# Kernel tuning notes

Measured on AMD Instinct MI355X. Metric: run time of the kernel, lower is better.

The kernel has to match this reference:

```python
import jax, jax.numpy as jnp
import numpy as np

B, N, D, H = 8, 1024, 768, 12
HD = D // H  # 64
SCALE = float(np.sqrt(HD))  # NOTE: source MULTIPLIES by sqrt(head_dim)


def setup_inputs() -> dict:
    key = jax.random.key(0)
    k1, k2, k3, k4 = jax.random.split(key, 4)
    x = jax.random.normal(k1, (B, N, D), dtype=jnp.float32)
    w_qkv = jax.random.normal(k2, (3 * D, D), dtype=jnp.float32) * (1.0 / np.sqrt(D))
    w_fc = jax.random.normal(k3, (D, D), dtype=jnp.float32) * (1.0 / np.sqrt(D))
    b_fc = jax.random.normal(k4, (D,), dtype=jnp.float32) * 0.01
    return {"x": x, "w_qkv": w_qkv, "w_fc": w_fc, "b_fc": b_fc}


def reference(x, w_qkv, w_fc, b_fc):
    b, n, d = x.shape
    # qkv projection (torch Linear: y = x @ W.T), no bias
    qkv = jnp.einsum('bnd,ed->bne', x, w_qkv)  # [b, n, 3*D]
    q, k, v = jnp.split(qkv, 3, axis=-1)
    # 'b n (h d) -> b h n d'
    to_heads = lambda t: t.reshape(b, n, H, HD).transpose(0, 2, 1, 3)
    q, k, v = map(to_heads, (q, k, v))
    # NOTE: faithful to source — scale MULTIPLIES and NO softmax is applied
    attn = SCALE * jnp.einsum('bhid,bhjd->bhij', q, k)  # [b, h, n, n]
    out = jnp.einsum('bhij,bhjd->bhid', attn, v)  # [b, h, n, hd]
    out = out.transpose(0, 2, 1, 3).reshape(b, n, H * HD)  # 'b h n d -> b n (h d)'
    out = jnp.einsum('bnd,ed->bne', out, w_fc) + b_fc  # fc (dropout = identity in eval)
    return out
```

## Files before the change

### kernel.cpp

```cpp
#include <hip/hip_runtime.h>
#include <stdint.h>

#define Bb 8
#define Nn 1024
#define Dd 768
#define Hh 12
#define HDd 64
#define Mm (Bb * Nn)
#define QKVN (3 * Dd)
#define SCALE_F 8.0f

typedef __attribute__((ext_vector_type(8))) short bf16x8;
typedef __attribute__((ext_vector_type(4))) float f32x4;

__device__ __forceinline__ float bf2f(unsigned short u) {
  unsigned int v = ((unsigned int)u) << 16;
  float f;
  __builtin_memcpy(&f, &v, 4);
  return f;
}
__device__ __forceinline__ unsigned short f2bf(float f) {
  unsigned int u;
  __builtin_memcpy(&u, &f, 4);
  u += 0x7FFFu + ((u >> 16) & 1u);
  return (unsigned short)(u >> 16);
}

#define GLDS16(g, l)                                                          \
  __builtin_amdgcn_global_load_lds(                                          \
      (const __attribute__((address_space(1))) void*)(g),                    \
      (__attribute__((address_space(3))) void*)(l), 16, 0, 0)

__global__ void convert_kernel(const float* __restrict__ x,
                               const float* __restrict__ wqkv,
                               const float* __restrict__ wfc,
                               unsigned short* __restrict__ xb,
                               unsigned short* __restrict__ wqkvb,
                               unsigned short* __restrict__ wfcb) {
  const int n1 = Mm * Dd / 4, n2 = QKVN * Dd / 4, n3 = Dd * Dd / 4;
  const int total = n1 + n2 + n3;
  for (int i = blockIdx.x * blockDim.x + threadIdx.x; i < total;
       i += gridDim.x * blockDim.x) {
    const float* src;
    unsigned short* dst;
    int j;
    if (i < n1) {
      src = x; dst = xb; j = i;
    } else if (i < n1 + n2) {
      src = wqkv; dst = wqkvb; j = i - n1;
    } else {
      src = wfc; dst = wfcb; j = i - n1 - n2;
    }
    const float4 v = ((const float4*)src)[j];
    ushort4 o;
    o.x = f2bf(v.x); o.y = f2bf(v.y); o.z = f2bf(v.z); o.w = f2bf(v.w);
    ((ushort4*)dst)[j] = o;
  }
}

template <int BM, bool BF16OUT>
__global__ __launch_bounds__(256, 4) void gemmk(
    const unsigned short* __restrict__ A, int lda, size_t aBatch,
    const unsigned short* __restrict__ Bm, int ldb, size_t bBatch,
    void* __restrict__ Cout, int ldc, size_t cBatch,
    const float* __restrict__ bias, int K) {
  constexpr int MI = BM / 32;
  constexpr int ACH = BM / 32;
  __shared__ unsigned short lds[(BM + 128) * 64];
  const int tid = threadIdx.x;
  const int lane = tid & 63, w = tid >> 6;

  const int gx = gridDim.x, gy = gridDim.y;
  int lid = blockIdx.x + gx * (blockIdx.y + gy * blockIdx.z);
  const int nwg = gx * gy * (int)gridDim.z;
  const int qch = nwg >> 3;
  lid = (lid & 7) * qch + (lid >> 3);
  const int bx = lid % gx;
  const int rem = lid / gx;
  const int by = rem % gy;
  const int bz = rem / gy;

  const int m0 = by * BM, n0 = bx * 128;
  const unsigned short* Aptr = A + (size_t)bz * aBatch;
  const unsigned short* Bptr = Bm + (size_t)bz * bBatch;

  const int lr = lane >> 3, lc = lane & 7;
  const int csw = (lc ^ lr) << 3;
  const int wr = w >> 1, wc = w & 1;
  const int fr = lane & 15, fk = lane >> 4;
  const int nt = K >> 6;

  f32x4 acc[MI][4] = {};

  for (int t = 0; t < nt; ++t) {
    const int k0 = t << 6;
#pragma unroll
    for (int l = 0; l < ACH; ++l) {
      const int c = w * ACH + l;
      GLDS16(Aptr + (size_t)(m0 + c * 8 + lr) * lda + k0 + csw,
             &lds[c * 512]);
    }
#pragma unroll
    for (int l = 0; l < 4; ++l) {
      const int c = w * 4 + l;
      GLDS16(Bptr + (size_t)(n0 + c * 8 + lr) * ldb + k0 + csw,
             &lds[BM * 64 + c * 512]);
    }
    __syncthreads();

#pragma unroll
    for (int ks = 0; ks < 2; ++ks) {
      bf16x8 af[MI], bf[4];
#pragma unroll
      for (int mi = 0; mi < MI; ++mi) {
        const int row = wr * (BM / 2) + mi * 16 + fr;
        af[mi] = *(const bf16x8*)&lds[row * 64 +
                                      ((ks * 32 + fk * 8) ^ ((row & 7) << 3))];
      }
#pragma unroll
      for (int ni = 0; ni < 4; ++ni) {
        const int row = wc * 64 + ni * 16 + fr;
        bf[ni] = *(const bf16x8*)&lds[BM * 64 + row * 64 +
                                      ((ks * 32 + fk * 8) ^ ((row & 7) << 3))];
      }
      __builtin_amdgcn_s_setprio(1);
#pragma unroll
      for (int mi = 0; mi < MI; ++mi)
#pragma unroll
        for (int ni = 0; ni < 4; ++ni)
          acc[mi][ni] = __builtin_amdgcn_mfma_f32_16x16x32_bf16(
              af[mi], bf[ni], acc[mi][ni], 0, 0, 0);
      __builtin_amdgcn_s_setprio(0);
    }
    __syncthreads();
  }

#pragma unroll
  for (int mi = 0; mi < MI; ++mi) {
#pragma unroll
    for (int ni = 0; ni < 4; ++ni) {
      const int col = n0 + wc * 64 + ni * 16 + fr;
      float bv = 0.0f;
      if (!BF16OUT) bv = bias[col];
#pragma unroll
      for (int r = 0; r < 4; ++r) {
        const int row = m0 + wr * (BM / 2) + mi * 16 + fk * 4 + r;
        const float val = acc[mi][ni][r] + bv;
        if (BF16OUT)
          ((unsigned short*)Cout + (size_t)bz * cBatch)
              [(size_t)row * ldc + col] = f2bf(val);
        else
          ((float*)Cout + (size_t)bz * cBatch)
              [(size_t)row * ldc + col] = val;
      }
    }
  }
}

__global__ __launch_bounds__(256) void ktv_kernel(
    const unsigned short* __restrict__ qkv, float* __restrict__ part) {
  __shared__ unsigned short kls[128 * 64];
  __shared__ unsigned short vls[128 * 64];
  const int bh = blockIdx.y;
  const int bb = bh / Hh, h = bh % Hh;
  const int chunk = blockIdx.x;
  const int j0 = chunk * 128;
  const int tid = threadIdx.x, lane = tid & 63, w = tid >> 6;
  const size_t rowbase = (size_t)(bb * Nn + j0);
#pragma unroll
  for (int i = 0; i < 4; ++i) {
    const int c = w * 4 + i;
    const int row = c * 8 + (lane >> 3);
    const int col = (lane & 7) * 8;
    const size_t g = (rowbase + row) * QKVN + h * HDd + col;
    GLDS16(qkv + g + Dd, &kls[c * 512]);
    GLDS16(qkv + g + 2 * Dd, &vls[c * 512]);
  }
  asm volatile("s_waitcnt vmcnt(0)" ::: "memory");
  __syncthreads();

  const int e0 = (tid >> 4) * 4, d0 = (tid & 15) * 4;
  float acc[4][4] = {};
#pragma unroll 4
  for (int j = 0; j < 128; ++j) {
    const ushort4 kv = *(const ushort4*)&kls[j * 64 + d0];
    const ushort4 vv = *(const ushort4*)&vls[j * 64 + e0];
    const float kf[4] = {bf2f(kv.x), bf2f(kv.y), bf2f(kv.z), bf2f(kv.w)};
    const float vf[4] = {bf2f(vv.x), bf2f(vv.y), bf2f(vv.z), bf2f(vv.w)};
#pragma unroll
    for (int e = 0; e < 4; ++e)
#pragma unroll
      for (int d = 0; d < 4; ++d) acc[e][d] += vf[e] * kf[d];
  }
  float* outp = part + ((size_t)chunk * 96 + bh) * 4096;
#pragma unroll
  for (int e = 0; e < 4; ++e)
#pragma unroll
    for (int d = 0; d < 4; ++d)
      outp[(e0 + e) * HDd + (d0 + d)] = acc[e][d];
}

__global__ __launch_bounds__(512) void w2_kernel(
    const float* __restrict__ part, const unsigned short* __restrict__ wfcb,
    unsigned short* __restrict__ w2t) {
  __shared__ unsigned short bt[64 * 72];
  const int h = blockIdx.x, b = blockIdx.y;
  const int tid = threadIdx.x, lane = tid & 63, w = tid >> 6;
  const float* kp = part + (size_t)(b * Hh + h) * 4096;
  for (int i = tid; i < 4096; i += 512) {
    float s = 0.0f;
#pragma unroll
    for (int cc = 0; cc < 8; ++cc) s += kp[(size_t)cc * 96 * 4096 + i];
    const int e = i >> 6, d = i & 63;
    bt[d * 72 + e] = f2bf(s * SCALE_F);
  }
  __syncthreads();
  const int fr = lane & 15, fk = lane >> 4;
  bf16x8 bfr[4][2];
#pragma unroll
  for (int ni = 0; ni < 4; ++ni)
#pragma unroll
    for (int ks = 0; ks < 2; ++ks)
      bfr[ni][ks] =
          *(const bf16x8*)&bt[(ni * 16 + fr) * 72 + ks * 32 + fk * 8];
  f32x4 acc[6][4] = {};
#pragma unroll
  for (int mi = 0; mi < 6; ++mi) {
    const int ep = w * 96 + mi * 16 + fr;
#pragma unroll
    for (int ks = 0; ks < 2; ++ks) {
      const bf16x8 af = *(const bf16x8*)&wfcb[(size_t)ep * Dd + h * HDd +
                                              ks * 32 + fk * 8];
#pragma unroll
      for (int ni = 0; ni < 4; ++ni)
        acc[mi][ni] = __builtin_amdgcn_mfma_f32_16x16x32_bf16(
            af, bfr[ni][ks], acc[mi][ni], 0, 0, 0);
    }
  }
  unsigned short* op = w2t + (size_t)b * Dd * Dd + h * HDd;
#pragma unroll
  for (int mi = 0; mi < 6; ++mi)
#pragma unroll
    for (int ni = 0; ni < 4; ++ni) {
      const int d = ni * 16 + fr;
      const int ep = w * 96 + mi * 16 + fk * 4;
#pragma unroll
      for (int r = 0; r < 4; ++r)
        op[(size_t)(ep + r) * Dd + d] = f2bf(acc[mi][ni][r]);
    }
}

extern "C" void kernel_launch(void* const* d_in, const int* in_sizes, int n_in,
                              void* d_out, int out_size, void* d_ws,
                              size_t ws_size, hipStream_t stream) {
  const float* x = (const float*)d_in[0];
  const float* wqkv = (const float*)d_in[1];
  const float* wfc = (const float*)d_in[2];
  const float* bfc = (const float*)d_in[3];
  float* out = (float*)d_out;

  char* ws = (char*)d_ws;
  unsigned short* xb    = (unsigned short*)(ws);
  float*          part  = (float*)(ws);
  unsigned short* wqkvb = (unsigned short*)(ws + 12582912);
  unsigned short* wfcb  = (unsigned short*)(ws + 16121856);
  unsigned short* qkv   = (unsigned short*)(ws + 17301504);
  unsigned short* w2t   = (unsigned short*)(ws + 56623104);

  convert_kernel<<<2112, 256, 0, stream>>>(x, wqkv, wfc, xb, wqkvb, wfcb);
  gemmk<128, true><<<dim3(QKVN / 128, Mm / 128, 1), 256, 0, stream>>>(
      xb, Dd, 0, wqkvb, Dd, 0, qkv, QKVN, 0, nullptr, Dd);
  ktv_kernel<<<dim3(8, 96), 256, 0, stream>>>(qkv, part);
  w2_kernel<<<dim3(Hh, Bb), 512, 0, stream>>>(part, wfcb, w2t);
  gemmk<64, false><<<dim3(Dd / 128, Nn / 64, Bb), 256, 0, stream>>>(
      qkv, QKVN, (size_t)Nn * QKVN, w2t, Dd, (size_t)Dd * Dd, out, Dd,
      (size_t)Nn * Dd, bfc, Dd);
}
```

Before: 95.20 us.

## Double-buffer GEMM LDS tiles with a K-step of 32 and prefetch

Splits the LDS into two buffers of BM+128 rows by 32 K elements each. The next K tile is issued with global-to-LDS loads while MFMAs run on the current tile, so each iteration now needs one barrier instead of two. This is meant to hide global load latency behind compute. In exchange the K step is halved, doubling the number of barrier rounds, and the XOR swizzle of the LDS layout is dropped, which can cause LDS bank conflicts on the fragment reads.

```diff
diff --git a/kernel.cpp b/kernel.cpp
--- a/kernel.cpp
+++ b/kernel.cpp
@@ -65,8 +65,9 @@
     void* __restrict__ Cout, int ldc, size_t cBatch,
     const float* __restrict__ bias, int K) {
   constexpr int MI = BM / 32;
-  constexpr int ACH = BM / 32;
-  __shared__ unsigned short lds[(BM + 128) * 64];
+  constexpr int ACH = BM / 64;
+  constexpr int SLOT = (BM + 128) * 32;
+  __shared__ unsigned short lds[2][SLOT];
   const int tid = threadIdx.x;
   const int lane = tid & 63, w = tid >> 6;
 
@@ -84,55 +85,59 @@
   const unsigned short* Aptr = A + (size_t)bz * aBatch;
   const unsigned short* Bptr = Bm + (size_t)bz * bBatch;
 
-  const int lr = lane >> 3, lc = lane & 7;
-  const int csw = (lc ^ lr) << 3;
+  const int sr = lane >> 2, sc = (lane & 3) * 8;
   const int wr = w >> 1, wc = w & 1;
   const int fr = lane & 15, fk = lane >> 4;
-  const int nt = K >> 6;
+  const int nt = K >> 5;
 
   f32x4 acc[MI][4] = {};
 
-  for (int t = 0; t < nt; ++t) {
-    const int k0 = t << 6;
+  auto stage = [&](int t, int s) {
+    const int k0 = t << 5;
 #pragma unroll
     for (int l = 0; l < ACH; ++l) {
       const int c = w * ACH + l;
-      GLDS16(Aptr + (size_t)(m0 + c * 8 + lr) * lda + k0 + csw,
-             &lds[c * 512]);
-    }
-#pragma unroll
-    for (int l = 0; l < 4; ++l) {
-      const int c = w * 4 + l;
-      GLDS16(Bptr + (size_t)(n0 + c * 8 + lr) * ldb + k0 + csw,
-             &lds[BM * 64 + c * 512]);
-    }
-    __syncthreads();
-
-#pragma unroll
-    for (int ks = 0; ks < 2; ++ks) {
-      bf16x8 af[MI], bf[4];
-#pragma unroll
-      for (int mi = 0; mi < MI; ++mi) {
-        const int row = wr * (BM / 2) + mi * 16 + fr;
-        af[mi] = *(const bf16x8*)&lds[row * 64 +
-                                      ((ks * 32 + fk * 8) ^ ((row & 7) << 3))];
-      }
-#pragma unroll
-      for (int ni = 0; ni < 4; ++ni) {
-        const int row = wc * 64 + ni * 16 + fr;
-        bf[ni] = *(const bf16x8*)&lds[BM * 64 + row * 64 +
-                                      ((ks * 32 + fk * 8) ^ ((row & 7) << 3))];
-      }
-      __builtin_amdgcn_s_setprio(1);
-#pragma unroll
-      for (int mi = 0; mi < MI; ++mi)
-#pragma unroll
-        for (int ni = 0; ni < 4; ++ni)
-          acc[mi][ni] = __builtin_amdgcn_mfma_f32_16x16x32_bf16(
-              af[mi], bf[ni], acc[mi][ni], 0, 0, 0);
-      __builtin_amdgcn_s_setprio(0);
-    }
-    __syncthreads();
+      GLDS16(Aptr + (size_t)(m0 + c * 16 + sr) * lda + k0 + sc,
+             &lds[s][c * 512]);
+    }
+#pragma unroll
+    for (int l = 0; l < 2; ++l) {
+      const int c = w * 2 + l;
+      GLDS16(Bptr + (size_t)(n0 + c * 16 + sr) * ldb + k0 + sc,
+             &lds[s][BM * 32 + c * 512]);
+    }
+  };
+
+  stage(0, 0);
+  asm volatile("s_waitcnt vmcnt(0)" ::: "memory");
+  __builtin_amdgcn_s_barrier();
+
+  for (int t = 0; t < nt; ++t) {
+    const int s = t & 1;
+    if (t + 1 < nt) stage(t + 1, s ^ 1);
+    bf16x8 af[MI], bf[4];
+#pragma unroll
+    for (int mi = 0; mi < MI; ++mi) {
+      const int row = wr * (BM / 2) + mi * 16 + fr;
+      af[mi] = *(const bf16x8*)&lds[s][row * 32 + fk * 8];
+    }
+#pragma unroll
+    for (int ni = 0; ni < 4; ++ni) {
+      const int row = wc * 64 + ni * 16 + fr;
+      bf[ni] = *(const bf16x8*)&lds[s][BM * 32 + row * 32 + fk * 8];
+    }
+    asm volatile("s_waitcnt lgkmcnt(0)" ::: "memory");
+    __builtin_amdgcn_sched_barrier(0);
+    __builtin_amdgcn_s_setprio(1);
+#pragma unroll
+    for (int mi = 0; mi < MI; ++mi)
+#pragma unroll
+      for (int ni = 0; ni < 4; ++ni)
+        acc[mi][ni] = __builtin_amdgcn_mfma_f32_16x16x32_bf16(
+            af[mi], bf[ni], acc[mi][ni], 0, 0, 0);
+    __builtin_amdgcn_s_setprio(0);
+    asm volatile("s_waitcnt vmcnt(0)" ::: "memory");
+    __builtin_amdgcn_s_barrier();
   }
 
 #pragma unroll
```

Result: slower. 105.2 us (+10.5%).

## Apply K^T V per head to Q then run shared FC GEMM

Applied to the files above, without the earlier changes.

Drops the per-batch fused weight W2 = Wfc·(KᵀV) and its batched GEMM. A new small kernel reduces the partial KᵀV sums to bf16. A second kernel multiplies Q by KᵀV per head and writes the result into the V slot of the qkv buffer. A single shared-weight GEMM over all rows with Wfc then produces the output. This avoids building eight 768x768 matrices and lets the final GEMM reuse one weight. It costs one extra launch, an intermediate round trip through global memory, and an extra bf16 rounding of the attention output.

```diff
diff --git a/kernel.cpp b/kernel.cpp
--- a/kernel.cpp
+++ b/kernel.cpp
@@ -200,54 +200,81 @@
       outp[(e0 + e) * HDd + (d0 + d)] = acc[e][d];
 }
 
-__global__ __launch_bounds__(512) void w2_kernel(
-    const float* __restrict__ part, const unsigned short* __restrict__ wfcb,
-    unsigned short* __restrict__ w2t) {
-  __shared__ unsigned short bt[64 * 72];
-  const int h = blockIdx.x, b = blockIdx.y;
+__global__ __launch_bounds__(256) void kfin_kernel(
+    const float* __restrict__ part, unsigned short* __restrict__ kfin) {
+  const int bh = blockIdx.x, tid = threadIdx.x;
+  const float* kp = part + (size_t)bh * 4096;
+  unsigned short* op = kfin + (size_t)bh * 4096;
+  for (int i = tid * 4; i < 4096; i += 1024) {
+    float4 s = {0.f, 0.f, 0.f, 0.f};
+#pragma unroll
+    for (int cc = 0; cc < 8; ++cc) {
+      const float4 v = *(const float4*)&kp[(size_t)cc * 96 * 4096 + i];
+      s.x += v.x; s.y += v.y; s.z += v.z; s.w += v.w;
+    }
+    ushort4 o;
+    o.x = f2bf(s.x * SCALE_F); o.y = f2bf(s.y * SCALE_F);
+    o.z = f2bf(s.z * SCALE_F); o.w = f2bf(s.w * SCALE_F);
+    *(ushort4*)&op[i] = o;
+  }
+}
+
+__global__ __launch_bounds__(256) void attn_out_kernel(
+    unsigned short* qkv, const unsigned short* __restrict__ kfin) {
+  __shared__ unsigned short qls[128 * 64];
+  __shared__ unsigned short bs[64 * 72];
+  const int bh = blockIdx.y;
+  const int bb = bh / Hh, h = bh % Hh;
+  const int jt = blockIdx.x;
   const int tid = threadIdx.x, lane = tid & 63, w = tid >> 6;
-  const float* kp = part + (size_t)(b * Hh + h) * 4096;
-  for (int i = tid; i < 4096; i += 512) {
-    float s = 0.0f;
-#pragma unroll
-    for (int cc = 0; cc < 8; ++cc) s += kp[(size_t)cc * 96 * 4096 + i];
+  const int lr = lane >> 3, lc = lane & 7;
+  const int csw = (lc ^ lr) << 3;
+  const size_t rowbase = (size_t)(bb * Nn + jt * 128);
+#pragma unroll
+  for (int l = 0; l < 4; ++l) {
+    const int c = w * 4 + l;
+    GLDS16(qkv + (rowbase + c * 8 + lr) * QKVN + h * HDd + csw,
+           &qls[c * 512]);
+  }
+  for (int i = tid * 8; i < 4096; i += 2048) {
     const int e = i >> 6, d = i & 63;
-    bt[d * 72 + e] = f2bf(s * SCALE_F);
-  }
+    *(bf16x8*)&bs[e * 72 + d] = *(const bf16x8*)&kfin[(size_t)bh * 4096 + i];
+  }
+  asm volatile("s_waitcnt vmcnt(0)" ::: "memory");
   __syncthreads();
+
   const int fr = lane & 15, fk = lane >> 4;
-  bf16x8 bfr[4][2];
-#pragma unroll
-  for (int ni = 0; ni < 4; ++ni)
-#pragma unroll
-    for (int ks = 0; ks < 2; ++ks)
-      bfr[ni][ks] =
-          *(const bf16x8*)&bt[(ni * 16 + fr) * 72 + ks * 32 + fk * 8];
-  f32x4 acc[6][4] = {};
-#pragma unroll
-  for (int mi = 0; mi < 6; ++mi) {
-    const int ep = w * 96 + mi * 16 + fr;
-#pragma unroll
-    for (int ks = 0; ks < 2; ++ks) {
-      const bf16x8 af = *(const bf16x8*)&wfcb[(size_t)ep * Dd + h * HDd +
-                                              ks * 32 + fk * 8];
-#pragma unroll
-      for (int ni = 0; ni < 4; ++ni)
+  f32x4 acc[2][4] = {};
+#pragma unroll
+  for (int ks = 0; ks < 2; ++ks) {
+    bf16x8 af[2];
+#pragma unroll
+    for (int mi = 0; mi < 2; ++mi) {
+      const int row = w * 32 + mi * 16 + fr;
+      af[mi] = *(const bf16x8*)&qls[row * 64 +
+                                    ((ks * 32 + fk * 8) ^ ((row & 7) << 3))];
+    }
+#pragma unroll
+    for (int ni = 0; ni < 4; ++ni) {
+      const bf16x8 bfr =
+          *(const bf16x8*)&bs[(ni * 16 + fr) * 72 + ks * 32 + fk * 8];
+#pragma unroll
+      for (int mi = 0; mi < 2; ++mi)
         acc[mi][ni] = __builtin_amdgcn_mfma_f32_16x16x32_bf16(
-            af, bfr[ni][ks], acc[mi][ni], 0, 0, 0);
-    }
-  }
-  unsigned short* op = w2t + (size_t)b * Dd * Dd + h * HDd;
-#pragma unroll
-  for (int mi = 0; mi < 6; ++mi)
-#pragma unroll
-    for (int ni = 0; ni < 4; ++ni) {
-      const int d = ni * 16 + fr;
-      const int ep = w * 96 + mi * 16 + fk * 4;
-#pragma unroll
-      for (int r = 0; r < 4; ++r)
-        op[(size_t)(ep + r) * Dd + d] = f2bf(acc[mi][ni][r]);
-    }
+            af[mi], bfr, acc[mi][ni], 0, 0, 0);
+    }
+  }
+#pragma unroll
+  for (int mi = 0; mi < 2; ++mi)
+#pragma unroll
+    for (int ni = 0; ni < 4; ++ni)
+#pragma unroll
+      for (int r = 0; r < 4; ++r) {
+        const int row = jt * 128 + w * 32 + mi * 16 + fk * 4 + r;
+        const int col = ni * 16 + fr;
+        qkv[((size_t)bb * Nn + row) * QKVN + 2 * Dd + h * HDd + col] =
+            f2bf(acc[mi][ni][r]);
+      }
 }
 
 extern "C" void kernel_launch(void* const* d_in, const int* in_sizes, int n_in,
@@ -265,14 +292,14 @@
   unsigned short* wqkvb = (unsigned short*)(ws + 12582912);
   unsigned short* wfcb  = (unsigned short*)(ws + 16121856);
   unsigned short* qkv   = (unsigned short*)(ws + 17301504);
-  unsigned short* w2t   = (unsigned short*)(ws + 56623104);
+  unsigned short* kfin  = (unsigned short*)(ws + 55050240);
 
   convert_kernel<<<2112, 256, 0, stream>>>(x, wqkv, wfc, xb, wqkvb, wfcb);
   gemmk<128, true><<<dim3(QKVN / 128, Mm / 128, 1), 256, 0, stream>>>(
       xb, Dd, 0, wqkvb, Dd, 0, qkv, QKVN, 0, nullptr, Dd);
   ktv_kernel<<<dim3(8, 96), 256, 0, stream>>>(qkv, part);
-  w2_kernel<<<dim3(Hh, Bb), 512, 0, stream>>>(part, wfcb, w2t);
-  gemmk<64, false><<<dim3(Dd / 128, Nn / 64, Bb), 256, 0, stream>>>(
-      qkv, QKVN, (size_t)Nn * QKVN, w2t, Dd, (size_t)Dd * Dd, out, Dd,
-      (size_t)Nn * Dd, bfc, Dd);
-}
+  kfin_kernel<<<96, 256, 0, stream>>>(part, kfin);
+  attn_out_kernel<<<dim3(8, 96), 256, 0, stream>>>(qkv, kfin);
+  gemmk<128, false><<<dim3(Dd / 128, Mm / 128, 1), 256, 0, stream>>>(
+      qkv + 2 * Dd, QKVN, 0, wfcb, Dd, 0, out, Dd, 0, bfc, Dd);
+}
```

New measurement: 96.86 us. No clear change (+1.8%).
